# Performance work log

Hardware: AMD Instinct MI355X
Metric: run time of the kernel (lower is better)

## Reference

```python
import jax, jax.numpy as jnp
import numpy as np

B, T, V, D, H = 256, 64, 6207, 512, 512  # batch, seq_len, vocab, emb_dim, hidden_dim
YF = 2048   # image feature dim -> concat with h (512) = 2560 gate input
EPS = 1e-10


def setup_inputs() -> dict:
    key = jax.random.key(0)
    ks = jax.random.split(key, 20)
    # torch init_parameters(): all params ~ U(-0.05, 0.05)
    u = lambda k, s: jax.random.uniform(k, s, jnp.float32, -0.05, 0.05)
    return {
        "y": jax.random.normal(ks[0], (B, YF), jnp.float32),
        "x": jax.random.randint(ks[1], (B, T), 0, V),
        "emb_w": u(ks[2], (V, D)),
        # bottom LSTM cell (input 512 -> hidden 512), torch layout: W_ih (4H, D)
        "W_ih": u(ks[3], (4 * H, D)), "W_hh": u(ks[4], (4 * H, H)),
        "b_ih": u(ks[5], (4 * H,)), "b_hh": u(ks[6], (4 * H,)),
        # top LSTM cell (input 512 -> hidden 512)
        "W_ih_t": u(ks[7], (4 * H, H)), "W_hh_t": u(ks[8], (4 * H, H)),
        "b_ih_t": u(ks[9], (4 * H,)), "b_hh_t": u(ks[10], (4 * H,)),
        # gate linear: Linear(2560, 512)
        "Wg": u(ks[11], (H, H + YF)), "bg": u(ks[12], (H,)),
        # final linear: Linear(512, 256)
        "Wlin": u(ks[13], (256, H)), "blin": u(ks[14], (256,)),
        # per-step gumbel-sigmoid uniforms (sampled inside forward in torch;
        # precomputed here so the reference is deterministic)
        "u1": jax.random.uniform(ks[15], (T, B, H), jnp.float32),
        "u2": jax.random.uniform(ks[16], (T, B, H), jnp.float32),
    }


def _lstm_cell(xt, h, c, Wi, Wh, bi, bh):
    # torch nn.LSTM gate order: i, f, g, o
    z = xt @ Wi.T + bi + h @ Wh.T + bh          # (B, 4H)
    i, f, g, o = jnp.split(z, 4, axis=-1)
    c = jax.nn.sigmoid(f) * c + jax.nn.sigmoid(i) * jnp.tanh(g)
    h = jax.nn.sigmoid(o) * jnp.tanh(c)
    return h, c


def reference(y, x, emb_w, W_ih, W_hh, b_ih, b_hh,
              W_ih_t, W_hh_t, b_ih_t, b_hh_t, Wg, bg, Wlin, blin, u1, u2):
    xs = jnp.transpose(emb_w[x], (1, 0, 2))     # (T, B, D)

    def step(carry, ins):
        h, c, ht, ct = carry
        xt, u1t, u2t = ins
        h, c = _lstm_cell(xt, h, c, W_ih, W_hh, b_ih, b_hh)
        # gate logits: relu(Linear([h, y]))
        logits = jax.nn.relu(jnp.concatenate([h, y], axis=1) @ Wg.T + bg)
        # custom gumbel-sigmoid noise: -log(log(U2+eps)/log(U1+eps)+eps)
        noise = -jnp.log(jnp.log(u2t + EPS) / jnp.log(u1t + EPS) + EPS)
        y_soft = jax.nn.sigmoid(logits + noise)
        # hard threshold at 0.5 with straight-through estimator
        y_hard = (y_soft >= 0.5).astype(y_soft.dtype)
        gate = y_hard - jax.lax.stop_gradient(y_soft) + y_soft
        hf = h * gate
        ht, ct = _lstm_cell(hf, ht, ct, W_ih_t, W_hh_t, b_ih_t, b_hh_t)
        return (h, c, ht, ct), None

    z0 = jnp.zeros((B, H), jnp.float32)
    (_, _, ht, _), _ = jax.lax.scan(step, (z0, z0, z0, z0), (xs, u1, u2))
    # dropout is identity in eval mode; torch output is (1, B, 256), squeezed here
    return jax.nn.relu(ht @ Wlin.T + blin)      # (B, 256)
```

## Files before the change

kernel.cpp:

```cpp
#include <hip/hip_runtime.h>
#include <hip/hip_bf16.h>


typedef __attribute__((ext_vector_type(8))) short short8;
typedef __attribute__((ext_vector_type(4))) float floatx4;
typedef __attribute__((ext_vector_type(4))) unsigned int uintx4;

#define MFMA16(a, b, c) __builtin_amdgcn_mfma_f32_16x16x32_bf16(a, b, c, 0, 0, 0)
#define AGENT __HIP_MEMORY_SCOPE_AGENT
#define HWREG_XCC_ID ((31u << 11) | (0u << 6) | 20u)

__device__ inline float bf2f(ushort u) {
    union { unsigned int u32; float f; } v; v.u32 = ((unsigned int)u) << 16; return v.f;
}
__device__ inline ushort f2bf(float f) {
    union { float f; unsigned int u; } v; v.f = f;
    return (ushort)((v.u + 0x7fffu + ((v.u >> 16) & 1u)) >> 16);
}
__device__ inline short8 ld8(const ushort* p) { return *(const short8*)p; }
__device__ inline float sigf(float x) { return 1.0f / (1.0f + expf(-x)); }
__device__ inline void mm3(floatx4& acc, short8 ah, short8 al, short8 bh, short8 bl) {
    acc = MFMA16(ah, bh, acc);
    acc = MFMA16(ah, bl, acc);
    acc = MFMA16(al, bh, acc);
}

__global__ __launch_bounds__(256) void k_prep(const float* __restrict__ w0,
                                              const float* __restrict__ w1,
                                              const float* __restrict__ w2,
                                              const float* __restrict__ w3,
                                              const float* __restrict__ wg,
                                              const float* __restrict__ wl,
                                              const float* __restrict__ em,
                                              const float* __restrict__ yy,
                                              ushort* __restrict__ wreg,
                                              uint* __restrict__ zbase) {
    unsigned i = blockIdx.x * 256u + threadIdx.x;
    if (i >= 9866784u) return;
    if (i >= 9338368u) {
        zbase[i - 9338368u] = 0u;
        return;
    }
    const float* src; ushort* hi; unsigned n, loc;
    if (i < 4194304u) {
        unsigned seg = i >> 20; loc = i & 1048575u; n = 1048576u;
        hi = wreg + seg * 2097152u;
        src = (seg == 0) ? w0 : (seg == 1) ? w1 : (seg == 2) ? w2 : w3;
    } else if (i < 5505024u) { loc = i - 4194304u; src = wg; hi = wreg + 8388608u;  n = 1310720u; }
    else if (i < 5636096u)   { loc = i - 5505024u; src = wl; hi = wreg + 11010048u; n = 131072u; }
    else if (i < 8814080u)   { loc = i - 5636096u; src = em; hi = wreg + 11272192u; n = 3177984u; }
    else                     { loc = i - 8814080u; src = yy; hi = wreg + 17628160u; n = 524288u; }
    float v = src[loc];
    ushort h = f2bf(v);
    hi[loc] = h;
    hi[n + loc] = f2bf(v - bf2f(h));
}

__global__ __launch_bounds__(512) void k_gy(const ushort* __restrict__ y_hi,
                                            const ushort* __restrict__ y_lo,
                                            const ushort* __restrict__ Wg_hi,
                                            const ushort* __restrict__ Wg_lo,
                                            const float* __restrict__ bg,
                                            float* __restrict__ gy) {
    __shared__ float zsB[4 * 528];
    int tid = threadIdx.x, lane = tid & 63, w = tid >> 6;
    int quad = lane >> 4, lr = lane & 15, q8 = quad * 8;
    int r0 = (blockIdx.x >> 4) * 16, n0 = (blockIdx.x & 15) * 32;
    int nh = w & 1, kq = w >> 1;
    int arow = r0 + lr, brow = n0 + nh * 16 + lr;
    floatx4 acc = {};
#pragma unroll
    for (int k0 = 0; k0 < 512; k0 += 32) {
        short8 ah = ld8(y_hi + arow * 2048 + kq * 512 + k0 + q8);
        short8 al = ld8(y_lo + arow * 2048 + kq * 512 + k0 + q8);
        short8 bh = ld8(Wg_hi + brow * 2560 + 512 + kq * 512 + k0 + q8);
        short8 bl = ld8(Wg_lo + brow * 2560 + 512 + kq * 512 + k0 + q8);
        mm3(acc, ah, al, bh, bl);
    }
#pragma unroll
    for (int r4 = 0; r4 < 4; r4++)
        zsB[kq * 528 + (quad * 4 + r4) * 33 + nh * 16 + lr] = acc[r4];
    __syncthreads();
    int ml = tid >> 5, jj = tid & 31;
    float s = zsB[ml * 33 + jj] + zsB[528 + ml * 33 + jj] +
              zsB[1056 + ml * 33 + jj] + zsB[1584 + ml * 33 + jj];
    gy[(r0 + ml) * 512 + n0 + jj] = s + bg[n0 + jj];
}

struct KP {
    const float *b_ih, *b_hh, *b_iht, *b_hht, *u1, *u2, *gy;
    const int* x;
    uint *hseq, *bseq, *tseq;
    uint* claim;
    uint *hP0, *hP1, *htP0, *htP1, *bitsP;
    ushort *ht_hi, *ht_lo;
    const ushort *Whh_hi, *Whh_lo, *Wih_hi, *Wih_lo;
    const ushort *Wiht_hi, *Wiht_lo, *Whht_hi, *Whht_lo;
    const ushort *Wg_hi, *Wg_lo, *em_hi, *em_lo;
};

__device__ inline void publish(uint* sq, uint v) {
    asm volatile("" ::: "memory");
    __builtin_amdgcn_s_waitcnt(0);
    __syncthreads();
    if (threadIdx.x == 0)
        __hip_atomic_store(sq, v, __ATOMIC_RELAXED, AGENT);
}
__device__ inline void poll16(const uint* sq, uint target) {
    if ((threadIdx.x >> 6) == 0) {
        int l = threadIdx.x & 63;
        for (;;) {
            uint v = (l < 16) ? __hip_atomic_load(&sq[l], __ATOMIC_RELAXED, AGENT) : target;
            if (__all((int)(v >= target))) break;
            __builtin_amdgcn_s_sleep(1);
        }
    }
    __syncthreads();
}

__device__ inline void issue_row16(const uint* __restrict__ src, int r0, uintx4* v) {
    int tid = threadIdx.x;
    int sr = tid >> 5, scol = (tid & 31) * 16;
    const uint* pp = src + (r0 + sr) * 512 + scol;
    asm volatile(
        "global_load_dwordx4 %0, %4, off sc0 sc1\n\t"
        "global_load_dwordx4 %1, %4, off offset:16 sc0 sc1\n\t"
        "global_load_dwordx4 %2, %4, off offset:32 sc0 sc1\n\t"
        "global_load_dwordx4 %3, %4, off offset:48 sc0 sc1"
        : "=v"(v[0]), "=v"(v[1]), "=v"(v[2]), "=v"(v[3])
        : "v"(pp) : "memory");
}
__device__ inline void unpack_row16(const uintx4* v, ushort* __restrict__ dst) {
    int tid = threadIdx.x;
    int sr = tid >> 5, scol = (tid & 31) * 16;
    ushort* d = dst + sr * 1032 + scol;
    union { uint u[4]; short8 s; } H0, H1, L0, L1;
    H0.u[0] = (v[0][0] & 0xffffu) | (v[0][1] << 16);
    H0.u[1] = (v[0][2] & 0xffffu) | (v[0][3] << 16);
    H0.u[2] = (v[1][0] & 0xffffu) | (v[1][1] << 16);
    H0.u[3] = (v[1][2] & 0xffffu) | (v[1][3] << 16);
    L0.u[0] = (v[0][0] >> 16) | (v[0][1] & 0xffff0000u);
    L0.u[1] = (v[0][2] >> 16) | (v[0][3] & 0xffff0000u);
    L0.u[2] = (v[1][0] >> 16) | (v[1][1] & 0xffff0000u);
    L0.u[3] = (v[1][2] >> 16) | (v[1][3] & 0xffff0000u);
    H1.u[0] = (v[2][0] & 0xffffu) | (v[2][1] << 16);
    H1.u[1] = (v[2][2] & 0xffffu) | (v[2][3] << 16);
    H1.u[2] = (v[3][0] & 0xffffu) | (v[3][1] << 16);
    H1.u[3] = (v[3][2] & 0xffffu) | (v[3][3] << 16);
    L1.u[0] = (v[2][0] >> 16) | (v[2][1] & 0xffff0000u);
    L1.u[1] = (v[2][2] >> 16) | (v[2][3] & 0xffff0000u);
    L1.u[2] = (v[3][0] >> 16) | (v[3][1] & 0xffff0000u);
    L1.u[3] = (v[3][2] >> 16) | (v[3][3] & 0xffff0000u);
    *(short8*)(d) = H0.s;
    *(short8*)(d + 8) = H1.s;
    *(short8*)(d + 520) = L0.s;
    *(short8*)(d + 520 + 8) = L1.s;
}

__device__ inline void stage_emb(const ushort* __restrict__ emh,
                                 const ushort* __restrict__ eml,
                                 const int* __restrict__ x, int r0, int t,
                                 ushort* __restrict__ dst) {
    int tid = threadIdx.x;
    int sr = tid >> 5, sc = (tid & 31) * 16;
    int tok = x[(r0 + sr) * 64 + t];
    const short8* ph = (const short8*)(emh + (size_t)tok * 512 + sc);
    const short8* pl = (const short8*)(eml + (size_t)tok * 512 + sc);
    short8 h0 = ph[0], h1 = ph[1], l0 = pl[0], l1 = pl[1];
    ushort* d = dst + sr * 1032;
    *(short8*)(d + sc) = h0;       *(short8*)(d + sc + 8) = h1;
    *(short8*)(d + 520 + sc) = l0; *(short8*)(d + 520 + sc + 8) = l1;
}

__device__ inline short8 fragA(const ushort* As, int row, int k) {
    return *(const short8*)(As + row * 1032 + k);
}

__global__ void __launch_bounds__(512, 1) k_main(KP p) {
    __shared__ ushort As[16 * 1032];
    __shared__ ushort Ae[16 * 1032];
    __shared__ ushort Az[16 * 1032];
    __shared__ ushort Ac[16 * 1032];
    __shared__ float zsD[4224];
    __shared__ uint gbits[256];
    __shared__ uint role_s;

    const int tid = threadIdx.x;
    const int w = tid >> 6;
    const int lane = tid & 63;
    const int quad = lane >> 4;
    const int lr = lane & 15;
    const int q8 = quad * 8;
    const float EPS = 1e-10f;

    if (tid == 0) {
        uint xcc = __builtin_amdgcn_s_getreg(HWREG_XCC_ID) & 7u;
        uint slot = __hip_atomic_fetch_add(&p.claim[xcc * 16], 1u,
                                           __ATOMIC_RELAXED, AGENT) & 31u;
        role_s = xcc * 32u + slot;
    }
    __syncthreads();
    const uint role = role_s;
    const int jb = (int)(role >> 4);
    const int g16 = (int)(role & 15u);
    const int r0 = g16 * 16, j0 = jb * 32;

    const int g4 = w & 3, team = w >> 2;
    const int gate = w >> 1, nh = w & 1;
    const int brow = gate * 512 + j0 + nh * 16 + lr;
    const int kq = w >> 1;
    const int browB = j0 + nh * 16 + lr;
    const int ml = tid >> 5, jj = tid & 31;

    const float biasAe0 = p.b_ih[j0 + jj]        + p.b_hh[j0 + jj];
    const float biasAe1 = p.b_ih[512 + j0 + jj]  + p.b_hh[512 + j0 + jj];
    const float biasAe2 = p.b_ih[1024 + j0 + jj] + p.b_hh[1024 + j0 + jj];
    const float biasAe3 = p.b_ih[1536 + j0 + jj] + p.b_hh[1536 + j0 + jj];
    const float biasCe0 = p.b_iht[j0 + jj]        + p.b_hht[j0 + jj];
    const float biasCe1 = p.b_iht[512 + j0 + jj]  + p.b_hht[512 + j0 + jj];
    const float biasCe2 = p.b_iht[1024 + j0 + jj] + p.b_hht[1024 + j0 + jj];
    const float biasCe3 = p.b_iht[1536 + j0 + jj] + p.b_hht[1536 + j0 + jj];
    const float gy_r = p.gy[(r0 + ml) * 512 + j0 + jj];

    const int rowA = g4 * 512 + j0 + lr;
    const ushort* WAh = (team ? p.Wih_hi : p.Whh_hi) + rowA * 512;
    const ushort* WAl = (team ? p.Wih_lo : p.Whh_lo) + rowA * 512;
    const ushort* WitH = p.Wiht_hi + brow * 512;
    const ushort* WitL = p.Wiht_lo + brow * 512;
    const ushort* WgH = p.Wg_hi + browB * 2560 + kq * 128;
    const ushort* WgL = p.Wg_lo + browB * 2560 + kq * 128;
    const float* pu1 = p.u1 + (r0 + ml) * 512 + j0 + jj;
    const float* pu2 = p.u2 + (r0 + ml) * 512 + j0 + jj;
    uint* hs = p.hseq + g16 * 16;
    uint* bs = p.bseq + g16 * 16;
    uint* hts = p.tseq + g16 * 16;

    short8 wHt[16], wLt[16];
    {
        const ushort* WhtH = p.Whht_hi + brow * 512;
        const ushort* WhtL = p.Whht_lo + brow * 512;
#pragma unroll
        for (int kk = 0; kk < 16; kk++) {
            wHt[kk] = ld8(WhtH + kk * 32 + q8);
            wLt[kk] = ld8(WhtL + kk * 32 + q8);
        }
    }

    for (int i = tid; i < 16 * 1032; i += 512) As[i] = 0;
    stage_emb(p.em_hi, p.em_lo, p.x, r0, 0, Ae);
    float U1 = __builtin_nontemporal_load(pu1);
    float U2 = __builtin_nontemporal_load(pu2);
    __syncthreads();

    float c_reg = 0.0f, ct_reg = 0.0f;

    for (int t = 0; t < 64; t++) {
        {
            const ushort* Ax = team ? Ae : As;
            floatx4 acc0 = {}, acc1 = {};
#pragma unroll
            for (int k0 = 0; k0 < 512; k0 += 32) {
                short8 xh = fragA(Ax, lr, k0 + q8);
                short8 xl = fragA(Ax, lr, 520 + k0 + q8);
                mm3(acc0, xh, xl, ld8(WAh + k0 + q8), ld8(WAl + k0 + q8));
                mm3(acc1, xh, xl, ld8(WAh + 8192 + k0 + q8), ld8(WAl + 8192 + k0 + q8));
            }
#pragma unroll
            for (int r4 = 0; r4 < 4; r4++) {
                zsD[team * 2112 + (quad * 4 + r4) * 132 + g4 * 32 + lr]      = acc0[r4];
                zsD[team * 2112 + (quad * 4 + r4) * 132 + g4 * 32 + 16 + lr] = acc1[r4];
            }
        }
        if (t > 0) poll16(hts, (uint)t); else __syncthreads();
        uintx4 vz[4];
        issue_row16((t & 1) ? p.htP0 : p.htP1, r0, vz);
        uint* hPcur = (t & 1) ? p.hP1 : p.hP0;
        {
            float zi = (zsD[ml * 132 + jj]      + zsD[2112 + ml * 132 + jj])      + biasAe0;
            float zf = (zsD[ml * 132 + 32 + jj] + zsD[2112 + ml * 132 + 32 + jj]) + biasAe1;
            float zg = (zsD[ml * 132 + 64 + jj] + zsD[2112 + ml * 132 + 64 + jj]) + biasAe2;
            float zo = (zsD[ml * 132 + 96 + jj] + zsD[2112 + ml * 132 + 96 + jj]) + biasAe3;
            c_reg = sigf(zf) * c_reg + sigf(zi) * tanhf(zg);
            float hv = sigf(zo) * tanhf(c_reg);
            ushort hb = f2bf(hv);
            ushort lb = f2bf(hv - bf2f(hb));
            __hip_atomic_store(&hPcur[(r0 + ml) * 512 + j0 + jj],
                               (uint)hb | ((uint)lb << 16), __ATOMIC_RELAXED, AGENT);
        }
        asm volatile("s_waitcnt vmcnt(0)" ::: "memory");
        __builtin_amdgcn_sched_barrier(0);
        __syncthreads();
        if (tid == 0)
            __hip_atomic_store(&hs[jb], (uint)(t + 1), __ATOMIC_RELAXED, AGENT);
        unpack_row16(vz, Az);
        float noise = -logf(logf(U2 + EPS) / logf(U1 + EPS) + EPS);
        __syncthreads();
        floatx4 c2acc = {};
#pragma unroll
        for (int kk = 0; kk < 6; kk++)
            mm3(c2acc, fragA(Az, lr, kk * 32 + q8), fragA(Az, lr, 520 + kk * 32 + q8),
                wHt[kk], wLt[kk]);
        poll16(hs, (uint)(t + 1));
        uintx4 va[4];
        issue_row16(hPcur, r0, va);
#pragma unroll
        for (int kk = 6; kk < 12; kk++)
            mm3(c2acc, fragA(Az, lr, kk * 32 + q8), fragA(Az, lr, 520 + kk * 32 + q8),
                wHt[kk], wLt[kk]);
        asm volatile("s_waitcnt vmcnt(0)" ::: "memory");
        __builtin_amdgcn_sched_barrier(0);
        unpack_row16(va, As);
        __syncthreads();

        {
            floatx4 acc = {};
#pragma unroll
            for (int k0 = 0; k0 < 128; k0 += 32)
                mm3(acc, fragA(As, lr, kq * 128 + k0 + q8),
                    fragA(As, lr, 520 + kq * 128 + k0 + q8),
                    ld8(WgH + k0 + q8), ld8(WgL + k0 + q8));
#pragma unroll
            for (int r4 = 0; r4 < 4; r4++)
                zsD[kq * 528 + (quad * 4 + r4) * 33 + nh * 16 + lr] = acc[r4];
        }
        __syncthreads();
        {
            float z2 = zsD[ml * 33 + jj] + zsD[528 + ml * 33 + jj] +
                       zsD[1056 + ml * 33 + jj] + zsD[1584 + ml * 33 + jj];
            float logit = fmaxf(z2 + gy_r, 0.0f);
            bool gbit = sigf(logit + noise) >= 0.5f;
            unsigned long long bm = __ballot((int)gbit);
            if ((lane & 31) == 0)
                __hip_atomic_store(&p.bitsP[(r0 + ml) * 16 + jb],
                                   (uint)(bm >> ((lane >> 5) * 32)),
                                   __ATOMIC_RELAXED, AGENT);
        }
        publish(&bs[jb], (uint)(t + 1));
        if (t < 63) stage_emb(p.em_hi, p.em_lo, p.x, r0, t + 1, Ae);
#pragma unroll
        for (int kk = 12; kk < 16; kk++)
            mm3(c2acc, fragA(Az, lr, kk * 32 + q8), fragA(Az, lr, 520 + kk * 32 + q8),
                wHt[kk], wLt[kk]);
#pragma unroll
        for (int r4 = 0; r4 < 4; r4++)
            zsD[2112 + (quad * 4 + r4) * 132 + gate * 32 + nh * 16 + lr] = c2acc[r4];
        poll16(bs, (uint)(t + 1));
        uint rb = 0;
        if (tid < 256)
            asm volatile("global_load_dword %0, %1, off sc0 sc1"
                         : "=v"(rb) : "v"(p.bitsP + r0 * 16 + tid) : "memory");
        if (t < 63) {
            U1 = __builtin_nontemporal_load(pu1 + (t + 1) * 131072);
            U2 = __builtin_nontemporal_load(pu2 + (t + 1) * 131072);
            asm volatile("s_waitcnt vmcnt(2)" ::: "memory");
        } else {
            asm volatile("s_waitcnt vmcnt(0)" ::: "memory");
        }
        __builtin_amdgcn_sched_barrier(0);
        if (tid < 256) gbits[tid] = rb;
        __syncthreads();
        {
            int sr = tid >> 5, sc = (tid & 31) * 16;
            uint word = gbits[sr * 16 + (sc >> 5)];
            uint chunk = (word >> (sc & 16)) & 0xffffu;
            const ushort* as0 = As + sr * 1032 + sc;
            ushort* ac0 = Ac + sr * 1032 + sc;
            union { uint u[4]; short8 s; } m0, m1;
#pragma unroll
            for (int j = 0; j < 4; j++) {
                uint b0 = 0u - ((chunk >> (2 * j)) & 1u);
                uint b1 = 0u - ((chunk >> (2 * j + 1)) & 1u);
                m0.u[j] = (b0 & 0xffffu) | (b1 << 16);
            }
#pragma unroll
            for (int j = 0; j < 4; j++) {
                uint b0 = 0u - ((chunk >> (8 + 2 * j)) & 1u);
                uint b1 = 0u - ((chunk >> (8 + 2 * j + 1)) & 1u);
                m1.u[j] = (b0 & 0xffffu) | (b1 << 16);
            }
            short8 h0 = *(const short8*)(as0);
            short8 h1 = *(const short8*)(as0 + 8);
            short8 l0 = *(const short8*)(as0 + 520);
            short8 l1 = *(const short8*)(as0 + 528);
            *(short8*)(ac0)       = h0 & m0.s;
            *(short8*)(ac0 + 8)   = h1 & m1.s;
            *(short8*)(ac0 + 520) = l0 & m0.s;
            *(short8*)(ac0 + 528) = l1 & m1.s;
        }
        __syncthreads();
        {
            floatx4 c1acc = {};
#pragma unroll
            for (int k0 = 0; k0 < 512; k0 += 32)
                mm3(c1acc, fragA(Ac, lr, k0 + q8), fragA(Ac, lr, 520 + k0 + q8),
                    ld8(WitH + k0 + q8), ld8(WitL + k0 + q8));
#pragma unroll
            for (int r4 = 0; r4 < 4; r4++)
                zsD[(quad * 4 + r4) * 132 + gate * 32 + nh * 16 + lr] = c1acc[r4];
        }
        __syncthreads();
        {
            float zi = (zsD[ml * 132 + jj]      + zsD[2112 + ml * 132 + jj])      + biasCe0;
            float zf = (zsD[ml * 132 + 32 + jj] + zsD[2112 + ml * 132 + 32 + jj]) + biasCe1;
            float zg = (zsD[ml * 132 + 64 + jj] + zsD[2112 + ml * 132 + 64 + jj]) + biasCe2;
            float zo = (zsD[ml * 132 + 96 + jj] + zsD[2112 + ml * 132 + 96 + jj]) + biasCe3;
            ct_reg = sigf(zf) * ct_reg + sigf(zi) * tanhf(zg);
            float hv = sigf(zo) * tanhf(ct_reg);
            ushort hb = f2bf(hv);
            ushort lb = f2bf(hv - bf2f(hb));
            int idx = (r0 + ml) * 512 + j0 + jj;
            uint* htcur = (t & 1) ? p.htP1 : p.htP0;
            __hip_atomic_store(&htcur[idx], (uint)hb | ((uint)lb << 16),
                               __ATOMIC_RELAXED, AGENT);
            if (t == 63) { p.ht_hi[idx] = hb; p.ht_lo[idx] = lb; }
        }
        publish(&hts[jb], (uint)(t + 1));
    }
}

__global__ __launch_bounds__(256) void k_final(const ushort* __restrict__ ht_hi,
                                               const ushort* __restrict__ ht_lo,
                                               const ushort* __restrict__ Wl_hi,
                                               const ushort* __restrict__ Wl_lo,
                                               const float* __restrict__ blin,
                                               float* __restrict__ out) {
    int tid = threadIdx.x, lane = tid & 63, w = tid >> 6;
    int wm = w & 1, wn = w >> 1, quad = lane >> 4, lr = lane & 15;
    int m0 = blockIdx.y * 64, n0 = blockIdx.x * 64;
    floatx4 acc[2][2] = {};
    for (int k0 = 0; k0 < 512; k0 += 32) {
        short8 ah[2], al[2], bh[2], bl[2];
#pragma unroll
        for (int tn = 0; tn < 2; tn++) {
            int n = n0 + wn * 32 + tn * 16 + lr;
            bh[tn] = ld8(Wl_hi + n * 512 + k0 + quad * 8);
            bl[tn] = ld8(Wl_lo + n * 512 + k0 + quad * 8);
        }
#pragma unroll
        for (int tm = 0; tm < 2; tm++) {
            int r = m0 + wm * 32 + tm * 16 + lr;
            ah[tm] = ld8(ht_hi + r * 512 + k0 + quad * 8);
            al[tm] = ld8(ht_lo + r * 512 + k0 + quad * 8);
        }
#pragma unroll
        for (int tm = 0; tm < 2; tm++)
#pragma unroll
            for (int tn = 0; tn < 2; tn++) mm3(acc[tm][tn], ah[tm], al[tm], bh[tn], bl[tn]);
    }
#pragma unroll
    for (int tm = 0; tm < 2; tm++)
#pragma unroll
        for (int tn = 0; tn < 2; tn++)
#pragma unroll
            for (int r4 = 0; r4 < 4; r4++) {
                int row = m0 + wm * 32 + tm * 16 + quad * 4 + r4;
                int n = n0 + wn * 32 + tn * 16 + lr;
                out[row * 256 + n] = fmaxf(acc[tm][tn][r4] + blin[n], 0.0f);
            }
}

extern "C" void kernel_launch(void* const* d_in, const int* in_sizes, int n_in,
                              void* d_out, int out_size, void* d_ws, size_t ws_size,
                              hipStream_t stream) {
    (void)in_sizes; (void)n_in; (void)out_size; (void)ws_size;
    const float* y      = (const float*)d_in[0];
    const int*   x      = (const int*)d_in[1];
    const float* emb    = (const float*)d_in[2];
    const float* W_ih   = (const float*)d_in[3];
    const float* W_hh   = (const float*)d_in[4];
    const float* b_ih   = (const float*)d_in[5];
    const float* b_hh   = (const float*)d_in[6];
    const float* W_iht  = (const float*)d_in[7];
    const float* W_hht  = (const float*)d_in[8];
    const float* b_iht  = (const float*)d_in[9];
    const float* b_hht  = (const float*)d_in[10];
    const float* Wg     = (const float*)d_in[11];
    const float* bg     = (const float*)d_in[12];
    const float* Wlin   = (const float*)d_in[13];
    const float* blin   = (const float*)d_in[14];
    const float* u1     = (const float*)d_in[15];
    const float* u2     = (const float*)d_in[16];
    float* out = (float*)d_out;

    uint* bar  = (uint*)d_ws;
    uint* hP0  = bar + 4128;
    uint* hP1  = hP0 + 131072;
    uint* htP0 = hP1 + 131072;
    uint* htP1 = htP0 + 131072;
    float* gy  = (float*)(htP1 + 131072);
    ushort* ht_hi = (ushort*)(gy + 131072);
    ushort* ht_lo = ht_hi + 131072;
    uint* bitsP = (uint*)(ht_lo + 131072);
    ushort* wreg = (ushort*)(bitsP + 4096);

    KP p;
    p.b_ih = b_ih; p.b_hh = b_hh; p.b_iht = b_iht; p.b_hht = b_hht;
    p.u1 = u1; p.u2 = u2; p.gy = gy; p.x = x;
    p.hseq = bar; p.bseq = bar + 256; p.tseq = bar + 512; p.claim = bar + 1024;
    p.hP0 = hP0; p.hP1 = hP1; p.htP0 = htP0; p.htP1 = htP1; p.bitsP = bitsP;
    p.ht_hi = ht_hi; p.ht_lo = ht_lo;
    p.Wih_hi  = wreg;             p.Wih_lo  = wreg + 1048576;
    p.Whh_hi  = wreg + 2097152;   p.Whh_lo  = wreg + 3145728;
    p.Wiht_hi = wreg + 4194304;   p.Wiht_lo = wreg + 5242880;
    p.Whht_hi = wreg + 6291456;   p.Whht_lo = wreg + 7340032;
    p.Wg_hi   = wreg + 8388608;   p.Wg_lo   = wreg + 9699328;
    p.em_hi   = wreg + 11272192;  p.em_lo   = wreg + 14450176;
    const ushort* Wl_hi = wreg + 11010048; const ushort* Wl_lo = wreg + 11141120;
    const ushort* y_hi  = wreg + 17628160; const ushort* y_lo  = wreg + 18152448;

    k_prep<<<dim3(38543), dim3(256), 0, stream>>>(W_ih, W_hh, W_iht, W_hht, Wg, Wlin,
                                                  emb, y, wreg, bar);
    k_gy<<<dim3(256), dim3(512), 0, stream>>>(y_hi, y_lo, p.Wg_hi, p.Wg_lo, bg, gy);

    void* args[] = {(void*)&p};
    hipLaunchCooperativeKernel((const void*)k_main, dim3(256), dim3(512), args, 0, stream);

    k_final<<<dim3(4, 4), dim3(256), 0, stream>>>(ht_hi, ht_lo, Wl_hi, Wl_lo, blin, out);
}
```

Before: 2.253 ms.

## Compute top-cell recurrent matmul upfront and publish top hidden state via vectorized stores

The top LSTM's recurrent h@W_hh contribution is no longer split into three chunks interleaved with the polls and the gate matmul. It is now computed in full before the first poll, and its partial sums are written to shared memory right away. The top hidden state is staged in shared memory and published by one wave using 16-byte stores with a single flag store, replacing 512 scattered per-element atomic stores. This is meant to cut global store transactions and flag latency on the critical path. The cost is an extra barrier and less overlap of the recurrent matmul with the wait on the peer state.

```diff
diff --git a/kernel.cpp b/kernel.cpp
--- a/kernel.cpp
+++ b/kernel.cpp
@@ -176,6 +176,16 @@
     return *(const short8*)(As + row * 1032 + k);
 }
 
+__device__ inline void pub_state(const uint* __restrict__ hx, uint* __restrict__ dst,
+                                 int r0, int j0, int lane) {
+    const uintx4* s = (const uintx4*)(hx + lane * 8);
+    uintx4 a = s[0], b = s[1];
+    uint* d = dst + (r0 + (lane >> 2)) * 512 + j0 + ((lane * 8) & 31);
+    asm volatile("global_store_dwordx4 %0, %1, off sc0 sc1\n\t"
+                 "global_store_dwordx4 %0, %2, off offset:16 sc0 sc1"
+                 :: "v"(d), "v"(a), "v"(b) : "memory");
+}
+
 __global__ void __launch_bounds__(512, 1) k_main(KP p) {
     __shared__ ushort As[16 * 1032];
     __shared__ ushort Ae[16 * 1032];
@@ -183,6 +193,7 @@
     __shared__ ushort Ac[16 * 1032];
     __shared__ float zsD[4224];
     __shared__ uint gbits[256];
+    __shared__ uint hx[512];
     __shared__ uint role_s;
 
     const int tid = threadIdx.x;
@@ -297,16 +308,15 @@
         __syncthreads();
         floatx4 c2acc = {};
 #pragma unroll
-        for (int kk = 0; kk < 6; kk++)
+        for (int kk = 0; kk < 16; kk++)
             mm3(c2acc, fragA(Az, lr, kk * 32 + q8), fragA(Az, lr, 520 + kk * 32 + q8),
                 wHt[kk], wLt[kk]);
+#pragma unroll
+        for (int r4 = 0; r4 < 4; r4++)
+            zsD[2112 + (quad * 4 + r4) * 132 + gate * 32 + nh * 16 + lr] = c2acc[r4];
         poll16(hs, (uint)(t + 1));
         uintx4 va[4];
         issue_row16(hPcur, r0, va);
-#pragma unroll
-        for (int kk = 6; kk < 12; kk++)
-            mm3(c2acc, fragA(Az, lr, kk * 32 + q8), fragA(Az, lr, 520 + kk * 32 + q8),
-                wHt[kk], wLt[kk]);
         asm volatile("s_waitcnt vmcnt(0)" ::: "memory");
         __builtin_amdgcn_sched_barrier(0);
         unpack_row16(va, As);
@@ -337,13 +347,6 @@
         }
         publish(&bs[jb], (uint)(t + 1));
         if (t < 63) stage_emb(p.em_hi, p.em_lo, p.x, r0, t + 1, Ae);
-#pragma unroll
-        for (int kk = 12; kk < 16; kk++)
-            mm3(c2acc, fragA(Az, lr, kk * 32 + q8), fragA(Az, lr, 520 + kk * 32 + q8),
-                wHt[kk], wLt[kk]);
-#pragma unroll
-        for (int r4 = 0; r4 < 4; r4++)
-            zsD[2112 + (quad * 4 + r4) * 132 + gate * 32 + nh * 16 + lr] = c2acc[r4];
         poll16(bs, (uint)(t + 1));
         uint rb = 0;
         if (tid < 256)
@@ -408,13 +411,20 @@
             float hv = sigf(zo) * tanhf(ct_reg);
             ushort hb = f2bf(hv);
             ushort lb = f2bf(hv - bf2f(hb));
-            int idx = (r0 + ml) * 512 + j0 + jj;
+            hx[ml * 32 + jj] = (uint)hb | ((uint)lb << 16);
+            if (t == 63) {
+                int idx = (r0 + ml) * 512 + j0 + jj;
+                p.ht_hi[idx] = hb; p.ht_lo[idx] = lb;
+            }
+        }
+        __syncthreads();
+        if (w == 0) {
             uint* htcur = (t & 1) ? p.htP1 : p.htP0;
-            __hip_atomic_store(&htcur[idx], (uint)hb | ((uint)lb << 16),
-                               __ATOMIC_RELAXED, AGENT);
-            if (t == 63) { p.ht_hi[idx] = hb; p.ht_lo[idx] = lb; }
-        }
-        publish(&hts[jb], (uint)(t + 1));
+            pub_state(hx, htcur, r0, j0, lane);
+            asm volatile("s_waitcnt vmcnt(0)" ::: "memory");
+            if (lane == 0)
+                __hip_atomic_store(&hts[jb], (uint)(t + 1), __ATOMIC_RELAXED, AGENT);
+        }
     }
 }
 
```

Measured after the change: 2.256 ms. No clear change (+0.1%).
